# Kernel optimization log

Measured on AMD Instinct MI355X. Metric: run time of the kernel, lower is better.

## Reference

```python
import jax, jax.numpy as jnp
import numpy as np

B, L, C = 4, 2048, 1024

def setup_inputs() -> dict:
    key = jax.random.key(0)
    k1, k2, k3 = jax.random.split(key, 3)
    net_in = jax.random.normal(k1, (B, L, C), dtype=jnp.float32)
    # torch Linear weights stored as (out, in); we keep that convention
    w_qkv = jax.random.normal(k2, (3 * C, C), dtype=jnp.float32) * (1.0 / np.sqrt(C))
    w_out = jax.random.normal(k3, (C, C), dtype=jnp.float32) * (1.0 / np.sqrt(C))
    return {"net_in": net_in, "w_qkv": w_qkv, "w_out": w_out}

def reference(net_in, w_qkv, w_out):
    Bc, Lc, Cc = net_in.shape
    qkv = jnp.einsum('blc,dc->bld', net_in, w_qkv)  # (B, L, 3C)
    q, k, v = jnp.split(qkv, 3, axis=-1)
    attn = jnp.einsum('bqc,bkc->bqk', q, k) / jnp.sqrt(jnp.float32(Cc))
    causal = jnp.tril(jnp.ones((Lc, Lc), dtype=bool))
    attn = jnp.where(causal[None, :, :], attn, -jnp.inf)
    attn = jax.nn.softmax(attn, axis=-1)
    out = jnp.einsum('bqk,bkc->bqc', attn, v)
    return jnp.einsum('blc,dc->bld', out, w_out)
```

## Files before the change

### kernel.cpp

```cpp
#include <hip/hip_runtime.h>
#include <hip/hip_bf16.h>
#include <cstdint>
#include <cstddef>

typedef __hip_bfloat16 bf16;
typedef float  floatx4 __attribute__((ext_vector_type(4)));
typedef __bf16 bf16x8  __attribute__((ext_vector_type(8)));

typedef __attribute__((address_space(1))) void as1_void;
typedef __attribute__((address_space(3))) void as3_void;

constexpr int Bn = 4, Ln = 2048, Cn = 1024;

__device__ __forceinline__ void store_one(float* p, float v) { *p = v; }
__device__ __forceinline__ void store_one(bf16*  p, float v) { *p = __float2bfloat16(v); }

#define BAR()    asm volatile("s_barrier" ::: "memory")
#define VMCNT2() asm volatile("s_waitcnt vmcnt(2)" ::: "memory")
#define VMCNT0() asm volatile("s_waitcnt vmcnt(0)" ::: "memory")
#define SCHEDB() __builtin_amdgcn_sched_barrier(0)
#define STAGE(gp, off) \
    __builtin_amdgcn_global_load_lds((const as1_void*)(gp), (as3_void*)(smem + (off)), 16, 0, 0)

__device__ __forceinline__ void gemm256_core(
    char* __restrict__ smem,
    const bf16* __restrict__ A, const bf16* __restrict__ B,
    int m0, int n0, int kbeg, int kend, int lda, int ldb,
    floatx4 (&acc)[8][4])
{
    const int tid  = threadIdx.x;
    const int lane = tid & 63;
    const int quad = lane >> 4;
    const int lr   = lane & 15;
    const int wave = tid >> 6;
    const int wm   = (wave >> 2) * 128;
    const int wn   = (wave & 3) * 64;

#pragma unroll
    for (int i = 0; i < 8; ++i)
#pragma unroll
        for (int j = 0; j < 4; ++j) { floatx4 z = {0.f, 0.f, 0.f, 0.f}; acc[i][j] = z; }

    const int srow = tid >> 3;
    const int sx   = (tid & 7) ^ (srow & 7);
    const bf16* gA = A + (size_t)(m0 + srow) * lda + sx * 8 + kbeg;
    const bf16* gB = B + (size_t)(n0 + srow) * ldb + sx * 8 + kbeg;
    const int wuni = __builtin_amdgcn_readfirstlane((tid & 0x1C0) * 16);

    const int aoff = (wm + lr) * 64;
    const int boff = (wn + lr) * 64;
    const int s0   = (quad ^ (lr & 7)) * 8;

    const int NT = (kend - kbeg) >> 6;

    STAGE(gB,             32768 + 0 * 8192 + wuni);
    STAGE(gB + 64  * ldb, 32768 + 1 * 8192 + wuni);
    STAGE(gB + 128 * ldb, 32768 + 2 * 8192 + wuni);
    STAGE(gB + 192 * ldb, 32768 + 3 * 8192 + wuni);
    STAGE(gA,                     0 * 8192 + wuni);
    STAGE(gA + 128 * lda,         2 * 8192 + wuni);
    STAGE(gA + 64  * lda,         1 * 8192 + wuni);
    STAGE(gA + 192 * lda,         3 * 8192 + wuni);
    VMCNT2();
    BAR();

#define LDA4(MB, SK) do { _Pragma("unroll") for (int ii = 0; ii < 4; ++ii) \
        a[ii] = *(const bf16x8*)(As + aoff + ((MB) * 4 + ii) * 1024 + (SK)); } while (0)
#define LDB4(SK) do { _Pragma("unroll") for (int nn = 0; nn < 4; ++nn) \
        b[nn] = *(const bf16x8*)(Bs + boff + nn * 1024 + (SK)); } while (0)
#define MFMA16(MB) do { _Pragma("unroll") for (int ii = 0; ii < 4; ++ii) { \
        _Pragma("unroll") for (int nn = 0; nn < 4; ++nn) \
            acc[(MB) * 4 + ii][nn] = __builtin_amdgcn_mfma_f32_16x16x32_bf16( \
                a[ii], b[nn], acc[(MB) * 4 + ii][nn], 0, 0, 0); } } while (0)

    for (int t = 0; t < NT; ++t) {
        const bf16* As = (const bf16*)(smem + (t & 1) * 65536);
        const bf16* Bs = (const bf16*)(smem + (t & 1) * 65536 + 32768);
        const int  wl  = ((t + 1) & 1) * 65536;
        const int  kn  = (t + 1) << 6;
        const bool more = (t + 1 < NT);
        bf16x8 a[4], b[4];

        LDB4(s0);
        LDA4(0, s0);
        if (more) {
            STAGE(gB + kn,            wl + 32768 + 0 * 8192 + wuni);
            STAGE(gB + kn + 64 * ldb, wl + 32768 + 1 * 8192 + wuni);
        }
        BAR(); SCHEDB();
        __builtin_amdgcn_s_setprio(1);
        MFMA16(0);
        __builtin_amdgcn_s_setprio(0);
        SCHEDB();
        if (more) VMCNT2(); else VMCNT0();
        BAR();

        LDA4(1, s0);
        if (more) {
            STAGE(gB + kn + 128 * ldb, wl + 32768 + 2 * 8192 + wuni);
            STAGE(gB + kn + 192 * ldb, wl + 32768 + 3 * 8192 + wuni);
        }
        BAR(); SCHEDB();
        __builtin_amdgcn_s_setprio(1);
        MFMA16(1);
        __builtin_amdgcn_s_setprio(0);
        SCHEDB();
        BAR();

        LDB4(s0 ^ 32);
        LDA4(0, s0 ^ 32);
        if (more) {
            STAGE(gA + kn,             wl + 0 * 8192 + wuni);
            STAGE(gA + kn + 128 * lda, wl + 2 * 8192 + wuni);
        }
        BAR(); SCHEDB();
        __builtin_amdgcn_s_setprio(1);
        MFMA16(0);
        __builtin_amdgcn_s_setprio(0);
        SCHEDB();
        BAR();

        LDA4(1, s0 ^ 32);
        if (more) {
            STAGE(gA + kn + 64  * lda, wl + 1 * 8192 + wuni);
            STAGE(gA + kn + 192 * lda, wl + 3 * 8192 + wuni);
        }
        BAR(); SCHEDB();
        __builtin_amdgcn_s_setprio(1);
        MFMA16(1);
        __builtin_amdgcn_s_setprio(0);
        SCHEDB();
        if (more) VMCNT2();
        BAR();
    }
#undef LDA4
#undef LDB4
#undef MFMA16
}

template <typename OutT>
__device__ __forceinline__ void gemm256(
    char* __restrict__ smem,
    const bf16* __restrict__ A, const bf16* __restrict__ B, OutT* __restrict__ C,
    int m0, int n0, int kbeg, int kend, int lda, int ldb, int ldc, float cscale)
{
    floatx4 acc[8][4];
    gemm256_core(smem, A, B, m0, n0, kbeg, kend, lda, ldb, acc);

    const int lane = threadIdx.x & 63;
    const int quad = lane >> 4;
    const int lr   = lane & 15;
    const int wave = threadIdx.x >> 6;
    const int wm   = (wave >> 2) * 128;
    const int wn   = (wave & 3) * 64;

#pragma unroll
    for (int mi = 0; mi < 8; ++mi) {
        const int row = m0 + wm + mi * 16 + quad * 4;
#pragma unroll
        for (int n = 0; n < 4; ++n) {
            const int col = n0 + wn + n * 16 + lr;
            OutT* cp = C + (size_t)row * ldc + col;
#pragma unroll
            for (int r = 0; r < 4; ++r)
                store_one(cp + (size_t)r * ldc, acc[mi][n][r] * cscale);
        }
    }
}

__device__ __forceinline__ void gemm_pv_128n(
    char* __restrict__ smem,
    const bf16* __restrict__ A, const bf16* __restrict__ B, float* __restrict__ C,
    int m0, int n0, int kend, int lda, int ldb, int ldc)
{
    const int tid  = threadIdx.x;
    const int lane = tid & 63;
    const int quad = lane >> 4;
    const int lr   = lane & 15;
    const int wave = tid >> 6;
    const int wm   = (wave >> 2) * 128;
    const int wn   = (wave & 3) * 32;

    floatx4 acc[8][2];
#pragma unroll
    for (int i = 0; i < 8; ++i)
#pragma unroll
        for (int j = 0; j < 2; ++j) { floatx4 z = {0.f, 0.f, 0.f, 0.f}; acc[i][j] = z; }

    const int srow = tid >> 3;
    const int sx   = (tid & 7) ^ (srow & 7);
    const bf16* gA = A + (size_t)(m0 + srow) * lda + sx * 8;
    const bf16* gB = B + (size_t)(n0 + srow) * ldb + sx * 8;
    const int wuni = __builtin_amdgcn_readfirstlane((tid & 0x1C0) * 16);

    const int aoff = (wm + lr) * 64;
    const int boff = (wn + lr) * 64;
    const int s0   = (quad ^ (lr & 7)) * 8;

    const int NT = kend >> 6;
    const int BUF = 49152;

    STAGE(gB,             32768 + 0 * 8192 + wuni);
    STAGE(gB + 64  * ldb, 32768 + 1 * 8192 + wuni);
    STAGE(gA,                     0 * 8192 + wuni);
    STAGE(gA + 128 * lda,         2 * 8192 + wuni);
    STAGE(gA + 64  * lda,         1 * 8192 + wuni);
    STAGE(gA + 192 * lda,         3 * 8192 + wuni);
    VMCNT2();
    BAR();

#define LDA4(MB, SK) do { _Pragma("unroll") for (int ii = 0; ii < 4; ++ii) \
        a[ii] = *(const bf16x8*)(As + aoff + ((MB) * 4 + ii) * 1024 + (SK)); } while (0)
#define LDB2(SK) do { _Pragma("unroll") for (int nn = 0; nn < 2; ++nn) \
        b[nn] = *(const bf16x8*)(Bs + boff + nn * 1024 + (SK)); } while (0)
#define MFMA8(MB) do { _Pragma("unroll") for (int ii = 0; ii < 4; ++ii) { \
        _Pragma("unroll") for (int nn = 0; nn < 2; ++nn) \
            acc[(MB) * 4 + ii][nn] = __builtin_amdgcn_mfma_f32_16x16x32_bf16( \
                a[ii], b[nn], acc[(MB) * 4 + ii][nn], 0, 0, 0); } } while (0)

    for (int t = 0; t < NT; ++t) {
        const bf16* As = (const bf16*)(smem + (t & 1) * BUF);
        const bf16* Bs = (const bf16*)(smem + (t & 1) * BUF + 32768);
        const int  wl  = ((t + 1) & 1) * BUF;
        const int  kn  = (t + 1) << 6;
        const bool more = (t + 1 < NT);
        bf16x8 a[4], b[2];

        LDB2(s0);
        LDA4(0, s0);
        if (more) {
            STAGE(gB + kn,            wl + 32768 + 0 * 8192 + wuni);
            STAGE(gB + kn + 64 * ldb, wl + 32768 + 1 * 8192 + wuni);
        }
        BAR(); SCHEDB();
        __builtin_amdgcn_s_setprio(1);
        MFMA8(0);
        __builtin_amdgcn_s_setprio(0);
        SCHEDB();
        if (more) VMCNT2(); else VMCNT0();
        BAR();

        LDA4(1, s0);
        if (more) {
            STAGE(gA + kn,             wl + 0 * 8192 + wuni);
            STAGE(gA + kn + 128 * lda, wl + 2 * 8192 + wuni);
        }
        BAR(); SCHEDB();
        __builtin_amdgcn_s_setprio(1);
        MFMA8(1);
        __builtin_amdgcn_s_setprio(0);
        SCHEDB();
        BAR();

        LDB2(s0 ^ 32);
        LDA4(0, s0 ^ 32);
        if (more) {
            STAGE(gA + kn + 64  * lda, wl + 1 * 8192 + wuni);
            STAGE(gA + kn + 192 * lda, wl + 3 * 8192 + wuni);
        }
        BAR(); SCHEDB();
        __builtin_amdgcn_s_setprio(1);
        MFMA8(0);
        __builtin_amdgcn_s_setprio(0);
        SCHEDB();
        BAR();

        LDA4(1, s0 ^ 32);
        BAR(); SCHEDB();
        __builtin_amdgcn_s_setprio(1);
        MFMA8(1);
        __builtin_amdgcn_s_setprio(0);
        SCHEDB();
        if (more) VMCNT2();
        BAR();
    }
#undef LDA4
#undef LDB2
#undef MFMA8

#pragma unroll
    for (int mi = 0; mi < 8; ++mi) {
        const int row = m0 + wm + mi * 16 + quad * 4;
#pragma unroll
        for (int n = 0; n < 2; ++n) {
            const int col = n0 + wn + n * 16 + lr;
            float* cp = C + (size_t)row * ldc + col;
#pragma unroll
            for (int r = 0; r < 4; ++r)
                cp[(size_t)r * ldc] = acc[mi][n][r];
        }
    }
}

__global__ __launch_bounds__(512, 2)
void g1_qk(const bf16* __restrict__ Xb, const bf16* __restrict__ Wqkb,
           bf16* __restrict__ QK)
{
    __shared__ __align__(16) char smem[131072];
    const int i = blockIdx.x;
    const int j = i >> 3;
    const int mt = (i & 7) * 4 + (j & 3);
    const int nt = j >> 2;
    gemm256<bf16>(smem, Xb, Wqkb, QK, mt * 256, nt * 256, 0, 1024, 1024, 1024, 2048, 1.0f);
}

__global__ __launch_bounds__(512, 2)
void g2_s_w2(const bf16* __restrict__ QK, const bf16* __restrict__ Wob,
             const bf16* __restrict__ WvT, bf16* __restrict__ S,
             bf16* __restrict__ W2)
{
    __shared__ __align__(16) char smem[131072];
    const int i = blockIdx.x;
    if (i < 144) {
        const int b = (i & 7) >> 1;
        const int t = (i >> 3) * 2 + (i & 1);
        int ti = (int)((sqrtf(8.f * t + 1.f) - 1.f) * 0.5f);
        while ((ti + 1) * (ti + 2) / 2 <= t) ++ti;
        while (ti * (ti + 1) / 2 > t) --ti;
        const int tj = t - ti * (ti + 1) / 2;
        const bf16* Aq = QK + (size_t)b * Ln * 2048;
        const bf16* Bk = Aq + 1024;
        bf16* Sb = S + (size_t)b * Ln * Ln;
        gemm256<bf16>(smem, Aq, Bk, Sb, ti * 256, tj * 256, 0, 1024, 2048, 2048, Ln, 0.03125f);
    } else {
        const int j = i - 144;
        gemm256<bf16>(smem, Wob, WvT, W2, (j & 3) * 256, (j >> 2) * 256, 0, 1024, 1024, 1024, 1024, 1.0f);
    }
}

__device__ __forceinline__ float waveMax(float x) {
#pragma unroll
    for (int o = 32; o > 0; o >>= 1) x = fmaxf(x, __shfl_xor(x, o, 64));
    return x;
}
__device__ __forceinline__ float waveSum(float x) {
#pragma unroll
    for (int o = 32; o > 0; o >>= 1) x += __shfl_xor(x, o, 64);
    return x;
}

__device__ void softmax_rows(bf16* __restrict__ S, int row0)
{
    const int wave = threadIdx.x >> 6, lane = threadIdx.x & 63;
    for (int it8 = 0; it8 < 8; ++it8) {
        const int row = row0 + wave * 8 + it8;
        const int q = row & (Ln - 1);
        bf16* Srow = S + (size_t)row * Ln;
        const int kmax = ((q >> 7) + 1) << 7;
        const int nv = (kmax + 511) >> 9;
        float x[4][8];
        float m = -1e30f;
        for (int it = 0; it < nv; ++it) {
            int c0 = it * 512 + lane * 8;
            bf16x8 v = *(const bf16x8*)(Srow + c0);
#pragma unroll
            for (int e = 0; e < 8; ++e) {
                float f = (float)v[e];
                f = (c0 + e <= q) ? f : -1e30f;
                x[it][e] = f;
                m = fmaxf(m, f);
            }
        }
        m = waveMax(m);
        float s = 0.f;
        for (int it = 0; it < nv; ++it)
#pragma unroll
            for (int e = 0; e < 8; ++e) {
                float ex = (x[it][e] > -1e29f) ? __expf(x[it][e] - m) : 0.f;
                x[it][e] = ex;
                s += ex;
            }
        s = waveSum(s);
        const float inv = 1.f / s;
        for (int it = 0; it < nv; ++it) {
            bf16x8 o;
#pragma unroll
            for (int e = 0; e < 8; ++e) o[e] = (__bf16)(x[it][e] * inv);
            *(bf16x8*)(Srow + it * 512 + lane * 8) = o;
        }
    }
}

__global__ __launch_bounds__(512, 2)
void g3_vwt_sm(const bf16* __restrict__ W2, const bf16* __restrict__ Xb,
               bf16* __restrict__ VWT, bf16* __restrict__ S)
{
    __shared__ __align__(16) char smem[131072];
    const int i = blockIdx.x;
    if (i < 128) {
        const int j = i >> 3;
        const int nt = (i & 7) * 4 + (j & 3);
        const int mt = j >> 2;
        gemm256<bf16>(smem, W2, Xb, VWT, mt * 256, nt * 256, 0, 1024, 1024, 1024, 8192, 1.0f);
    } else {
        softmax_rows(S, (i - 128) * 64);
    }
}

__global__ __launch_bounds__(512, 2)
void g4_out(const bf16* __restrict__ P, const bf16* __restrict__ VWT,
            float* __restrict__ out)
{
    __shared__ __align__(16) char smem[98304];
    const int i = blockIdx.x;
    const int r = i & 7;
    const int b = r >> 1, p = r & 1;
    const int q = i >> 3;
    const int nt = p * 4 + (q & 3);
    const int mt = q >> 2;

    const bf16* Pp = P + (size_t)b * Ln * Ln;
    const bf16* Bv = VWT + (size_t)b * Ln;
    float* Co = out + (size_t)b * Ln * Cn;
    gemm_pv_128n(smem, Pp, Bv, Co, mt * 256, nt * 128, (mt + 1) * 256, Ln, 8192, Cn);
}

__global__ __launch_bounds__(256)
void cast_all(const float* __restrict__ X, const float* __restrict__ Wqkv,
              const float* __restrict__ Wo,
              bf16* __restrict__ Xb, bf16* __restrict__ Wqkb,
              bf16* __restrict__ Wob, bf16* __restrict__ WvT)
{
    int blk = blockIdx.x;
    if (blk < 11264) {
        int i = blk * 256 + threadIdx.x;
        const float* src; bf16* dst; int off;
        if (i < 2097152)                 { src = X;    dst = Xb;   off = i; }
        else if (i < 2097152 + 524288)   { src = Wqkv; dst = Wqkb; off = i - 2097152; }
        else                             { src = Wo;   dst = Wob;  off = i - 2621440; }
        float4 f = ((const float4*)src)[off];
        bf16 o0 = __float2bfloat16(f.x), o1 = __float2bfloat16(f.y);
        bf16 o2 = __float2bfloat16(f.z), o3 = __float2bfloat16(f.w);
        ushort4 u;
        u.x = *(unsigned short*)&o0; u.y = *(unsigned short*)&o1;
        u.z = *(unsigned short*)&o2; u.w = *(unsigned short*)&o3;
        *(ushort4*)(dst + (size_t)off * 4) = u;
    } else {
        __shared__ float t[32][33];
        int tt = blk - 11264;
        int c0 = (tt & 31) * 32;
        int r0 = (tt >> 5) * 32;
        const float* Wv = Wqkv + 2048 * 1024;
        int xcol = threadIdx.x & 31, y0 = threadIdx.x >> 5;
#pragma unroll
        for (int p = 0; p < 4; ++p) {
            int y = y0 + 8 * p;
            t[y][xcol] = Wv[(size_t)(r0 + y) * 1024 + c0 + xcol];
        }
        __syncthreads();
#pragma unroll
        for (int p = 0; p < 4; ++p) {
            int mloc = y0 + 8 * p;
            WvT[(size_t)(c0 + mloc) * 1024 + r0 + xcol] = __float2bfloat16(t[xcol][mloc]);
        }
    }
}

extern "C" void kernel_launch(void* const* d_in, const int* in_sizes, int n_in,
                              void* d_out, int out_size, void* d_ws, size_t ws_size,
                              hipStream_t stream)
{
    const float* X    = (const float*)d_in[0];
    const float* Wqkv = (const float*)d_in[1];
    const float* Wout = (const float*)d_in[2];
    float* out = (float*)d_out;

    char* ws = (char*)d_ws;
    const size_t MiB = 1024ull * 1024ull;
    bf16* Xb   = (bf16*)(ws + 0);
    bf16* QK   = (bf16*)(ws + 16 * MiB);
    bf16* VWT  = (bf16*)(ws + 48 * MiB);
    bf16* Sbuf = (bf16*)(ws + 64 * MiB);
    bf16* Wqkb = (bf16*)(ws + 96 * MiB);
    bf16* WvT  = (bf16*)(ws + 100 * MiB);
    bf16* Wob  = (bf16*)(ws + 102 * MiB);
    bf16* W2   = (bf16*)(ws + 104 * MiB);

    cast_all<<<dim3(12288), 256, 0, stream>>>(X, Wqkv, Wout, Xb, Wqkb, Wob, WvT);

    g1_qk<<<dim3(256), 512, 0, stream>>>(Xb, Wqkb, QK);

    g2_s_w2<<<dim3(160), 512, 0, stream>>>(QK, Wob, WvT, Sbuf, W2);

    g3_vwt_sm<<<dim3(256), 512, 0, stream>>>(W2, Xb, VWT, Sbuf);

    g4_out<<<dim3(256), 512, 0, stream>>>(Sbuf, VWT, out);
}
```

Measured before the change: 224.0 us.

## Shrink GEMM tiles to 128 rows and pair causal PV tiles for load balance

```diff
diff --git a/kernel.cpp b/kernel.cpp
--- a/kernel.cpp
+++ b/kernel.cpp
@@ -168,9 +168,9 @@
     }
 }
 
-__device__ __forceinline__ void gemm_pv_128n(
+__device__ __forceinline__ void gemm_m128n256(
     char* __restrict__ smem,
-    const bf16* __restrict__ A, const bf16* __restrict__ B, float* __restrict__ C,
+    const bf16* __restrict__ A, const bf16* __restrict__ B, bf16* __restrict__ C,
     int m0, int n0, int kend, int lda, int ldb, int ldc)
 {
     const int tid  = threadIdx.x;
@@ -178,14 +178,14 @@
     const int quad = lane >> 4;
     const int lr   = lane & 15;
     const int wave = tid >> 6;
-    const int wm   = (wave >> 2) * 128;
-    const int wn   = (wave & 3) * 32;
-
-    floatx4 acc[8][2];
-#pragma unroll
-    for (int i = 0; i < 8; ++i)
-#pragma unroll
-        for (int j = 0; j < 2; ++j) { floatx4 z = {0.f, 0.f, 0.f, 0.f}; acc[i][j] = z; }
+    const int wm   = (wave >> 2) * 64;
+    const int wn   = (wave & 3) * 64;
+
+    floatx4 acc[4][4];
+#pragma unroll
+    for (int i = 0; i < 4; ++i)
+#pragma unroll
+        for (int j = 0; j < 4; ++j) { floatx4 z = {0.f, 0.f, 0.f, 0.f}; acc[i][j] = z; }
 
     const int srow = tid >> 3;
     const int sx   = (tid & 7) ^ (srow & 7);
@@ -197,89 +197,205 @@
     const int boff = (wn + lr) * 64;
     const int s0   = (quad ^ (lr & 7)) * 8;
 
-    const int NT = kend >> 6;
+    const int NT  = kend >> 6;
     const int BUF = 49152;
 
-    STAGE(gB,             32768 + 0 * 8192 + wuni);
-    STAGE(gB + 64  * ldb, 32768 + 1 * 8192 + wuni);
-    STAGE(gA,                     0 * 8192 + wuni);
-    STAGE(gA + 128 * lda,         2 * 8192 + wuni);
-    STAGE(gA + 64  * lda,         1 * 8192 + wuni);
-    STAGE(gA + 192 * lda,         3 * 8192 + wuni);
-    VMCNT2();
+    STAGE(gA,             0 * 8192 + wuni);
+    STAGE(gA + 64 * lda,  1 * 8192 + wuni);
+    STAGE(gB,             16384 + 0 * 8192 + wuni);
+    STAGE(gB + 64  * ldb, 16384 + 1 * 8192 + wuni);
+    STAGE(gB + 128 * ldb, 16384 + 2 * 8192 + wuni);
+    STAGE(gB + 192 * ldb, 16384 + 3 * 8192 + wuni);
+    VMCNT0();
     BAR();
 
-#define LDA4(MB, SK) do { _Pragma("unroll") for (int ii = 0; ii < 4; ++ii) \
-        a[ii] = *(const bf16x8*)(As + aoff + ((MB) * 4 + ii) * 1024 + (SK)); } while (0)
-#define LDB2(SK) do { _Pragma("unroll") for (int nn = 0; nn < 2; ++nn) \
+#define LDA2(PH, SK) do { _Pragma("unroll") for (int ii = 0; ii < 2; ++ii) \
+        a[ii] = *(const bf16x8*)(As + aoff + ((PH) * 2 + ii) * 1024 + (SK)); } while (0)
+#define LDB4(SK) do { _Pragma("unroll") for (int nn = 0; nn < 4; ++nn) \
         b[nn] = *(const bf16x8*)(Bs + boff + nn * 1024 + (SK)); } while (0)
-#define MFMA8(MB) do { _Pragma("unroll") for (int ii = 0; ii < 4; ++ii) { \
-        _Pragma("unroll") for (int nn = 0; nn < 2; ++nn) \
-            acc[(MB) * 4 + ii][nn] = __builtin_amdgcn_mfma_f32_16x16x32_bf16( \
-                a[ii], b[nn], acc[(MB) * 4 + ii][nn], 0, 0, 0); } } while (0)
+#define MFMA8(PH) do { _Pragma("unroll") for (int ii = 0; ii < 2; ++ii) { \
+        _Pragma("unroll") for (int nn = 0; nn < 4; ++nn) \
+            acc[(PH) * 2 + ii][nn] = __builtin_amdgcn_mfma_f32_16x16x32_bf16( \
+                a[ii], b[nn], acc[(PH) * 2 + ii][nn], 0, 0, 0); } } while (0)
 
     for (int t = 0; t < NT; ++t) {
         const bf16* As = (const bf16*)(smem + (t & 1) * BUF);
-        const bf16* Bs = (const bf16*)(smem + (t & 1) * BUF + 32768);
+        const bf16* Bs = (const bf16*)(smem + (t & 1) * BUF + 16384);
         const int  wl  = ((t + 1) & 1) * BUF;
         const int  kn  = (t + 1) << 6;
         const bool more = (t + 1 < NT);
-        bf16x8 a[4], b[2];
+        bf16x8 a[2], b[4];
+
+        LDB4(s0);
+        LDA2(0, s0);
+        if (more) {
+            STAGE(gB + kn,            wl + 16384 + 0 * 8192 + wuni);
+            STAGE(gB + kn + 64 * ldb, wl + 16384 + 1 * 8192 + wuni);
+        }
+        BAR(); SCHEDB();
+        __builtin_amdgcn_s_setprio(1);
+        MFMA8(0);
+        __builtin_amdgcn_s_setprio(0);
+        SCHEDB();
+        BAR();
+
+        LDA2(1, s0);
+        if (more) {
+            STAGE(gB + kn + 128 * ldb, wl + 16384 + 2 * 8192 + wuni);
+            STAGE(gB + kn + 192 * ldb, wl + 16384 + 3 * 8192 + wuni);
+        }
+        BAR(); SCHEDB();
+        __builtin_amdgcn_s_setprio(1);
+        MFMA8(1);
+        __builtin_amdgcn_s_setprio(0);
+        SCHEDB();
+        BAR();
+
+        LDB4(s0 ^ 32);
+        LDA2(0, s0 ^ 32);
+        if (more) {
+            STAGE(gA + kn,            wl + 0 * 8192 + wuni);
+            STAGE(gA + kn + 64 * lda, wl + 1 * 8192 + wuni);
+        }
+        BAR(); SCHEDB();
+        __builtin_amdgcn_s_setprio(1);
+        MFMA8(0);
+        __builtin_amdgcn_s_setprio(0);
+        SCHEDB();
+        BAR();
+
+        LDA2(1, s0 ^ 32);
+        BAR(); SCHEDB();
+        __builtin_amdgcn_s_setprio(1);
+        MFMA8(1);
+        __builtin_amdgcn_s_setprio(0);
+        SCHEDB();
+        if (more) VMCNT0();
+        BAR();
+    }
+#undef LDA2
+#undef LDB4
+#undef MFMA8
+
+#pragma unroll
+    for (int mi = 0; mi < 4; ++mi) {
+        const int row = m0 + wm + mi * 16 + quad * 4;
+#pragma unroll
+        for (int n = 0; n < 4; ++n) {
+            const int col = n0 + wn + n * 16 + lr;
+            bf16* cp = C + (size_t)row * ldc + col;
+#pragma unroll
+            for (int r = 0; r < 4; ++r)
+                store_one(cp + (size_t)r * ldc, acc[mi][n][r]);
+        }
+    }
+}
+
+__device__ __forceinline__ void gemm_m128n128(
+    char* __restrict__ smem,
+    const bf16* __restrict__ A, const bf16* __restrict__ B, float* __restrict__ C,
+    int m0, int n0, int kend, int lda, int ldb, int ldc)
+{
+    const int tid  = threadIdx.x;
+    const int lane = tid & 63;
+    const int quad = lane >> 4;
+    const int lr   = lane & 15;
+    const int wave = tid >> 6;
+    const int wm   = (wave >> 2) * 64;
+    const int wn   = (wave & 3) * 32;
+
+    floatx4 acc[4][2];
+#pragma unroll
+    for (int i = 0; i < 4; ++i)
+#pragma unroll
+        for (int j = 0; j < 2; ++j) { floatx4 z = {0.f, 0.f, 0.f, 0.f}; acc[i][j] = z; }
+
+    const int srow = tid >> 3;
+    const int sx   = (tid & 7) ^ (srow & 7);
+    const bf16* gA = A + (size_t)(m0 + srow) * lda + sx * 8;
+    const bf16* gB = B + (size_t)(n0 + srow) * ldb + sx * 8;
+    const int wuni = __builtin_amdgcn_readfirstlane((tid & 0x1C0) * 16);
+
+    const int aoff = (wm + lr) * 64;
+    const int boff = (wn + lr) * 64;
+    const int s0   = (quad ^ (lr & 7)) * 8;
+
+    const int NT  = kend >> 6;
+    const int BUF = 32768;
+
+    STAGE(gA,            0 * 8192 + wuni);
+    STAGE(gA + 64 * lda, 1 * 8192 + wuni);
+    STAGE(gB,            16384 + 0 * 8192 + wuni);
+    STAGE(gB + 64 * ldb, 16384 + 1 * 8192 + wuni);
+    VMCNT0();
+    BAR();
+
+#define LDA2(PH, SK) do { _Pragma("unroll") for (int ii = 0; ii < 2; ++ii) \
+        a[ii] = *(const bf16x8*)(As + aoff + ((PH) * 2 + ii) * 1024 + (SK)); } while (0)
+#define LDB2(SK) do { _Pragma("unroll") for (int nn = 0; nn < 2; ++nn) \
+        b[nn] = *(const bf16x8*)(Bs + boff + nn * 1024 + (SK)); } while (0)
+#define MFMA4(PH) do { _Pragma("unroll") for (int ii = 0; ii < 2; ++ii) { \
+        _Pragma("unroll") for (int nn = 0; nn < 2; ++nn) \
+            acc[(PH) * 2 + ii][nn] = __builtin_amdgcn_mfma_f32_16x16x32_bf16( \
+                a[ii], b[nn], acc[(PH) * 2 + ii][nn], 0, 0, 0); } } while (0)
+
+    for (int t = 0; t < NT; ++t) {
+        const bf16* As = (const bf16*)(smem + (t & 1) * BUF);
+        const bf16* Bs = (const bf16*)(smem + (t & 1) * BUF + 16384);
+        const int  wl  = ((t + 1) & 1) * BUF;
+        const int  kn  = (t + 1) << 6;
+        const bool more = (t + 1 < NT);
+        bf16x8 a[2], b[2];
 
         LDB2(s0);
-        LDA4(0, s0);
-        if (more) {
-            STAGE(gB + kn,            wl + 32768 + 0 * 8192 + wuni);
-            STAGE(gB + kn + 64 * ldb, wl + 32768 + 1 * 8192 + wuni);
-        }
-        BAR(); SCHEDB();
-        __builtin_amdgcn_s_setprio(1);
-        MFMA8(0);
-        __builtin_amdgcn_s_setprio(0);
-        SCHEDB();
-        if (more) VMCNT2(); else VMCNT0();
-        BAR();
-
-        LDA4(1, s0);
-        if (more) {
-            STAGE(gA + kn,             wl + 0 * 8192 + wuni);
-            STAGE(gA + kn + 128 * lda, wl + 2 * 8192 + wuni);
-        }
-        BAR(); SCHEDB();
-        __builtin_amdgcn_s_setprio(1);
-        MFMA8(1);
+        LDA2(0, s0);
+        if (more) {
+            STAGE(gB + kn,            wl + 16384 + 0 * 8192 + wuni);
+            STAGE(gB + kn + 64 * ldb, wl + 16384 + 1 * 8192 + wuni);
+        }
+        BAR(); SCHEDB();
+        __builtin_amdgcn_s_setprio(1);
+        MFMA4(0);
+        __builtin_amdgcn_s_setprio(0);
+        SCHEDB();
+        BAR();
+
+        LDA2(1, s0);
+        if (more) {
+            STAGE(gA + kn,            wl + 0 * 8192 + wuni);
+            STAGE(gA + kn + 64 * lda, wl + 1 * 8192 + wuni);
+        }
+        BAR(); SCHEDB();
+        __builtin_amdgcn_s_setprio(1);
+        MFMA4(1);
         __builtin_amdgcn_s_setprio(0);
         SCHEDB();
         BAR();
 
         LDB2(s0 ^ 32);
-        LDA4(0, s0 ^ 32);
-        if (more) {
-            STAGE(gA + kn + 64  * lda, wl + 1 * 8192 + wuni);
-            STAGE(gA + kn + 192 * lda, wl + 3 * 8192 + wuni);
-        }
-        BAR(); SCHEDB();
-        __builtin_amdgcn_s_setprio(1);
-        MFMA8(0);
-        __builtin_amdgcn_s_setprio(0);
-        SCHEDB();
-        BAR();
-
-        LDA4(1, s0 ^ 32);
-        BAR(); SCHEDB();
-        __builtin_amdgcn_s_setprio(1);
-        MFMA8(1);
-        __builtin_amdgcn_s_setprio(0);
-        SCHEDB();
-        if (more) VMCNT2();
-        BAR();
-    }
-#undef LDA4
+        LDA2(0, s0 ^ 32);
+        BAR(); SCHEDB();
+        __builtin_amdgcn_s_setprio(1);
+        MFMA4(0);
+        __builtin_amdgcn_s_setprio(0);
+        SCHEDB();
+        BAR();
+
+        LDA2(1, s0 ^ 32);
+        BAR(); SCHEDB();
+        __builtin_amdgcn_s_setprio(1);
+        MFMA4(1);
+        __builtin_amdgcn_s_setprio(0);
+        SCHEDB();
+        if (more) VMCNT0();
+        BAR();
+    }
+#undef LDA2
 #undef LDB2
-#undef MFMA8
-
-#pragma unroll
-    for (int mi = 0; mi < 8; ++mi) {
+#undef MFMA4
+
+#pragma unroll
+    for (int mi = 0; mi < 4; ++mi) {
         const int row = m0 + wm + mi * 16 + quad * 4;
 #pragma unroll
         for (int n = 0; n < 2; ++n) {
@@ -339,11 +455,11 @@
     return x;
 }
 
-__device__ void softmax_rows(bf16* __restrict__ S, int row0)
+__device__ void softmax_rows32(bf16* __restrict__ S, int row0)
 {
     const int wave = threadIdx.x >> 6, lane = threadIdx.x & 63;
-    for (int it8 = 0; it8 < 8; ++it8) {
-        const int row = row0 + wave * 8 + it8;
+    for (int it4 = 0; it4 < 4; ++it4) {
+        const int row = row0 + wave * 4 + it4;
         const int q = row & (Ln - 1);
         bf16* Srow = S + (size_t)row * Ln;
         const int kmax = ((q >> 7) + 1) << 7;
@@ -385,34 +501,34 @@
 void g3_vwt_sm(const bf16* __restrict__ W2, const bf16* __restrict__ Xb,
                bf16* __restrict__ VWT, bf16* __restrict__ S)
 {
-    __shared__ __align__(16) char smem[131072];
+    __shared__ __align__(16) char smem[98304];
     const int i = blockIdx.x;
-    if (i < 128) {
-        const int j = i >> 3;
-        const int nt = (i & 7) * 4 + (j & 3);
-        const int mt = j >> 2;
-        gemm256<bf16>(smem, W2, Xb, VWT, mt * 256, nt * 256, 0, 1024, 1024, 1024, 8192, 1.0f);
-    } else {
-        softmax_rows(S, (i - 128) * 64);
-    }
+    const int j = i >> 3;
+    const int nt = (i & 7) * 4 + (j & 3);
+    const int mh = j >> 2;
+    gemm_m128n256(smem, W2, Xb, VWT, mh * 128, nt * 256, 1024, 1024, 1024, 8192);
+    softmax_rows32(S, i * 32);
 }
 
 __global__ __launch_bounds__(512, 2)
 void g4_out(const bf16* __restrict__ P, const bf16* __restrict__ VWT,
             float* __restrict__ out)
 {
-    __shared__ __align__(16) char smem[98304];
+    __shared__ __align__(16) char smem[65536];
     const int i = blockIdx.x;
     const int r = i & 7;
     const int b = r >> 1, p = r & 1;
     const int q = i >> 3;
     const int nt = p * 4 + (q & 3);
-    const int mt = q >> 2;
+    const int mh = q >> 2;
 
     const bf16* Pp = P + (size_t)b * Ln * Ln;
     const bf16* Bv = VWT + (size_t)b * Ln;
     float* Co = out + (size_t)b * Ln * Cn;
-    gemm_pv_128n(smem, Pp, Bv, Co, mt * 256, nt * 128, (mt + 1) * 256, Ln, 8192, Cn);
+    const int n0 = nt * 128;
+
+    gemm_m128n128(smem, Pp, Bv, Co, (15 - mh) * 128, n0, (16 - mh) * 128, Ln, 8192, Cn);
+    gemm_m128n128(smem, Pp, Bv, Co, mh * 128,        n0, (mh + 1) * 128,  Ln, 8192, Cn);
 }
 
 __global__ __launch_bounds__(256)
```

After: 224.1 us. No clear change (+0.0%).
